# Performance work log

Hardware: AMD Instinct MI355X
Metric: run time of the kernel (lower is better)

Reference implementation:

```python
import jax, jax.numpy as jnp
import numpy as np

E = 2048
H = 16
DH = E // H  # 128
B, T = 2, 2048
EPS = 1e-8


def rmsnorm(x, g):
    rms = jnp.sqrt(jnp.mean(x * x, axis=-1, keepdims=True) + EPS)
    return g * (x / rms)


def setup_inputs() -> dict:
    key = jax.random.key(0)
    ks = jax.random.split(key, 16)
    s_in = 1.0 / np.sqrt(E)
    s_ff = 1.0 / np.sqrt(4 * E)
    return {
        "x": jax.random.normal(ks[0], (B, T, E), dtype=jnp.float32),
        # stacked per-head QKV projections, stored (in, out) so y = x @ W + b
        "wq": jax.random.normal(ks[1], (H, E, DH), dtype=jnp.float32) * s_in,
        "bq": jax.random.normal(ks[2], (H, DH), dtype=jnp.float32) * s_in,
        "wk": jax.random.normal(ks[3], (H, E, DH), dtype=jnp.float32) * s_in,
        "bk": jax.random.normal(ks[4], (H, DH), dtype=jnp.float32) * s_in,
        "wv": jax.random.normal(ks[5], (H, E, DH), dtype=jnp.float32) * s_in,
        "bv": jax.random.normal(ks[6], (H, DH), dtype=jnp.float32) * s_in,
        "wo": jax.random.normal(ks[7], (E, E), dtype=jnp.float32) * s_in,
        "bo": jax.random.normal(ks[8], (E,), dtype=jnp.float32) * s_in,
        "w1": jax.random.normal(ks[9], (E, 4 * E), dtype=jnp.float32) * s_in,
        "b1": jax.random.normal(ks[10], (4 * E,), dtype=jnp.float32) * s_in,
        "w2": jax.random.normal(ks[11], (4 * E, E), dtype=jnp.float32) * s_ff,
        "b2": jax.random.normal(ks[12], (E,), dtype=jnp.float32) * s_ff,
        "g1": jnp.ones((E,), dtype=jnp.float32),
        "g2": jnp.ones((E,), dtype=jnp.float32),
    }


def reference(x, wq, bq, wk, bk, wv, bv, wo, bo, w1, b1, w2, b2, g1, g2):
    b, t, e = x.shape
    # --- attention sublayer ---
    h = rmsnorm(x, g1)
    q = jnp.einsum("bte,hed->bhtd", h, wq) + bq[None, :, None, :]
    k = jnp.einsum("bte,hed->bhtd", h, wk) + bk[None, :, None, :]
    v = jnp.einsum("bte,hed->bhtd", h, wv) + bv[None, :, None, :]
    scores = jnp.einsum("bhtd,bhsd->bhts", q, k) / jnp.sqrt(jnp.float32(DH))
    causal = jnp.tril(jnp.ones((t, t), dtype=bool))
    scores = jnp.where(causal[None, None], scores, -jnp.inf)
    w = jax.nn.softmax(scores, axis=-1)
    o = jnp.einsum("bhts,bhsd->bhtd", w, v)
    o = o.transpose(0, 2, 1, 3).reshape(b, t, e)  # concat heads on last dim
    x = x + o @ wo + bo
    # --- FFN sublayer (exact GELU, dropout is identity at inference) ---
    h = rmsnorm(x, g2)
    x = x + jax.nn.gelu(h @ w1 + b1, approximate=False) @ w2 + b2
    return x
```

## Files before the change

kernel.cpp:

```cpp
#include <hip/hip_runtime.h>
#include <hip/hip_bf16.h>

typedef unsigned short u16;
typedef unsigned int   u32;
typedef __attribute__((ext_vector_type(8))) short short8;
typedef __attribute__((ext_vector_type(4))) float f32x4;
typedef __attribute__((ext_vector_type(4))) unsigned short u16x4;

#define E_    2048
#define H_    16
#define DH_   128
#define B_    2
#define T_    2048
#define NTOK  4096
#define QKVN  6144

#define VMCNT(n) asm volatile("s_waitcnt vmcnt(" #n ")" ::: "memory")
#define LGKM0()  asm volatile("s_waitcnt lgkmcnt(0)" ::: "memory")

__device__ __forceinline__ u16 f2bf(float f) {
  union { float f; u32 u; } v; v.f = f;
  u32 r = (v.u + 0x7FFFu + ((v.u >> 16) & 1u)) >> 16;
  return (u16)r;
}

__global__ __launch_bounds__(256) void tr64(
    const float* __restrict__ in, u16* __restrict__ out,
    int R, int C, size_t inZ, size_t outZ)
{
  __shared__ float t[64][65];
  const float* ib = in + (size_t)blockIdx.z * inZ;
  u16* ob = out + (size_t)blockIdx.z * outZ;
  const int r0 = blockIdx.y * 64, c0 = blockIdx.x * 64;
  const int tid = threadIdx.x;
  const int rr = tid >> 4;
  const int cc = (tid & 15) * 4;
  #pragma unroll
  for (int p = 0; p < 4; ++p) {
    const float4 v = *(const float4*)(ib + (size_t)(r0 + p * 16 + rr) * C + c0 + cc);
    t[cc + 0][p * 16 + rr] = v.x;
    t[cc + 1][p * 16 + rr] = v.y;
    t[cc + 2][p * 16 + rr] = v.z;
    t[cc + 3][p * 16 + rr] = v.w;
  }
  __syncthreads();
  const int wr = tid >> 3;
  const int wc = (tid & 7) * 8;
  #pragma unroll
  for (int p = 0; p < 2; ++p) {
    short8 s;
    #pragma unroll
    for (int j = 0; j < 8; ++j) s[j] = (short)f2bf(t[p * 32 + wr][wc + j]);
    *(short8*)(ob + (size_t)(c0 + p * 32 + wr) * R + r0 + wc) = s;
  }
}

__global__ __launch_bounds__(256) void bias_cat(
    const float* __restrict__ bq, const float* __restrict__ bk,
    const float* __restrict__ bv, float* __restrict__ bias)
{
  int idx = blockIdx.x * 256 + threadIdx.x;
  const float* bb = (idx < 2048) ? bq : (idx < 4096) ? bk : bv;
  bias[idx] = bb[idx & 2047];
}

__global__ __launch_bounds__(256) void rmsnorm_k(
    const float* __restrict__ x, const float* __restrict__ g, u16* __restrict__ o)
{
  const int row = blockIdx.x;
  const float4* xr = (const float4*)(x + (size_t)row * E_);
  const float4* gr = (const float4*)g;
  const int tid = threadIdx.x;
  float4 a0 = xr[tid], a1 = xr[tid + 256];
  float s = a0.x*a0.x + a0.y*a0.y + a0.z*a0.z + a0.w*a0.w
          + a1.x*a1.x + a1.y*a1.y + a1.z*a1.z + a1.w*a1.w;
  #pragma unroll
  for (int m = 1; m < 64; m <<= 1) s += __shfl_xor(s, m);
  __shared__ float wsum[4];
  if ((tid & 63) == 0) wsum[tid >> 6] = s;
  __syncthreads();
  float tot = wsum[0] + wsum[1] + wsum[2] + wsum[3];
  float rinv = rsqrtf(tot * (1.0f / E_) + 1e-8f);
  float4 g0 = gr[tid], g1 = gr[tid + 256];
  u16x4 o0, o1;
  o0[0] = f2bf(a0.x * g0.x * rinv); o0[1] = f2bf(a0.y * g0.y * rinv);
  o0[2] = f2bf(a0.z * g0.z * rinv); o0[3] = f2bf(a0.w * g0.w * rinv);
  o1[0] = f2bf(a1.x * g1.x * rinv); o1[1] = f2bf(a1.y * g1.y * rinv);
  o1[2] = f2bf(a1.z * g1.z * rinv); o1[3] = f2bf(a1.w * g1.w * rinv);
  u16x4* orow = (u16x4*)(o + (size_t)row * E_);
  orow[tid] = o0;
  orow[tid + 256] = o1;
}

__device__ __forceinline__ void gload_lds16(const void* g, u16* lds_base) {
  __builtin_amdgcn_global_load_lds(
      (const __attribute__((address_space(1))) u32*)g,
      (__attribute__((address_space(3))) u32*)lds_base, 16, 0, 0);
}

template<int BM, int BN, int MODE, int EPI>
__global__ __launch_bounds__(512, 2)
void gemm3(const u16* __restrict__ A, const u16* __restrict__ Bt,
           const float* __restrict__ bias, const float* __restrict__ resid,
           void* __restrict__ out, u16* __restrict__ vtout, int M, int N, int K)
{
  constexpr int WROWS = BM / 2;
  constexpr int WCOLS = BN / 4;
  constexpr int MR    = WROWS / 16;
  constexpr int BUF   = (BM + BN) * 32;
  __shared__ __align__(16) u16 sh[3 * BUF];

  const int tid  = threadIdx.x;
  const int lane = tid & 63;
  const int l15  = lane & 15, lg = lane >> 4;
  const int w    = tid >> 6;
  const int wm   = w >> 2;
  const int wn   = w & 3;
  const int xs   = (l15 >> 1) & 3;

  const int nbx = N / BN;
  const int xcd = blockIdx.x & 7, j = blockIdx.x >> 3;
  int m0, n0;
  if constexpr (MODE == 1) {
    const int ncx = nbx >> 3;
    n0 = (xcd * ncx + j % ncx) * BN;
    m0 = (j / ncx) * BM;
  } else {
    const int nwg = nbx * (M / BM);
    const int sid = xcd * (nwg >> 3) + j;
    m0 = (sid / nbx) * BM;
    n0 = (sid % nbx) * BN;
  }

  const int r0 = tid >> 2;
  const int c0 = (((tid & 3) ^ ((tid >> 3) & 3)) * 8);
  const u16* gA  = A  + (size_t)(m0 + r0) * K + c0;
  const u16* gB  = Bt + (size_t)(n0 + r0) * K + c0;
  const u16* gA2 = gA + (size_t)128 * K;
  const u16* gB2 = gB + (size_t)128 * K;
  const int wub = (tid & ~63) * 8;

  f32x4 acc[MR][4] = {};
  const int NT = K >> 5;

  #pragma unroll
  for (int t = 0; t < 2; ++t) {
    u16* wb = sh + t * BUF;
    const int kS = t * 32;
    if constexpr (BM == 256) {
      gload_lds16(gA  + kS, wb + wub);
      gload_lds16(gA2 + kS, wb + 4096 + wub);
      gload_lds16(gB  + kS, wb + 8192 + wub);
      gload_lds16(gB2 + kS, wb + 12288 + wub);
    } else {
      gload_lds16(gA  + kS, wb + wub);
      gload_lds16(gB  + kS, wb + 4096 + wub);
      gload_lds16(gB2 + kS, wb + 8192 + wub);
    }
  }
  if constexpr (BM == 256) VMCNT(4); else VMCNT(3);
  __builtin_amdgcn_s_barrier();

  int i = 0;

#define KTILE(CUR, STG)                                                          \
  do {                                                                           \
    const u16* rb = sh + (CUR) * BUF;                                            \
    u16* wb = sh + (STG) * BUF;                                                  \
    const bool st = (i + 2 < NT);                                                \
    const int kS = (i + 2) << 5;                                                 \
    const int rem = NT - 1 - i;                                                  \
    if (st) {                                                                    \
      if constexpr (BM == 256) {                                                 \
        gload_lds16(gA  + kS, wb + wub);                                         \
        gload_lds16(gA2 + kS, wb + 4096 + wub);                                  \
        gload_lds16(gB  + kS, wb + 8192 + wub);                                  \
        gload_lds16(gB2 + kS, wb + 12288 + wub);                                 \
      } else {                                                                   \
        gload_lds16(gA  + kS, wb + wub);                                         \
        gload_lds16(gB  + kS, wb + 4096 + wub);                                  \
        gload_lds16(gB2 + kS, wb + 8192 + wub);                                  \
      }                                                                          \
    }                                                                            \
    short8 bf[4];                                                                \
    _Pragma("unroll")                                                            \
    for (int n = 0; n < 4; ++n)                                                  \
      bf[n] = *(const short8*)(rb + BM * 32 + (wn * WCOLS + n * 16 + l15) * 32 + ((lg ^ xs) * 8)); \
    _Pragma("unroll")                                                            \
    for (int mh = 0; mh < MR / 4; ++mh) {                                        \
      short8 af[4];                                                              \
      _Pragma("unroll")                                                          \
      for (int m = 0; m < 4; ++m)                                                \
        af[m] = *(const short8*)(rb + (wm * WROWS + (mh * 4 + m) * 16 + l15) * 32 + ((lg ^ xs) * 8)); \
      _Pragma("unroll")                                                          \
      for (int m = 0; m < 4; ++m)                                                \
        _Pragma("unroll")                                                        \
        for (int n = 0; n < 4; ++n)                                              \
          acc[mh * 4 + m][n] = __builtin_amdgcn_mfma_f32_16x16x32_bf16(af[m], bf[n], acc[mh * 4 + m][n], 0, 0, 0); \
    }                                                                            \
    if (rem >= 2) { if constexpr (BM == 256) { VMCNT(4); } else { VMCNT(3); } }  \
    else { VMCNT(0); }                                                           \
    __builtin_amdgcn_s_barrier();                                                \
    ++i;                                                                         \
  } while (0)

  const int trips = NT / 3;
  #pragma unroll 1
  for (int t = 0; t < trips; ++t) {
    KTILE(0, 2);
    KTILE(1, 0);
    KTILE(2, 1);
  }
  if (i < NT) KTILE(0, 2);
  if (i < NT) KTILE(1, 0);
#undef KTILE

  float bv[4];
  #pragma unroll
  for (int n = 0; n < 4; ++n) bv[n] = bias[n0 + wn * WCOLS + n * 16 + l15];

  if constexpr (EPI == 1) {
    #pragma unroll
    for (int n = 0; n < 4; ++n) {
      const int col = n0 + wn * WCOLS + n * 16 + l15;
      #pragma unroll
      for (int m = 0; m < MR; ++m)
        #pragma unroll
        for (int r = 0; r < 4; ++r) {
          const int row = m0 + wm * WROWS + m * 16 + lg * 4 + r;
          const size_t off = (size_t)row * N + col;
          ((float*)out)[off] = acc[m][n][r] + bv[n] + resid[off];
        }
    }
  } else if (EPI == 3 && n0 >= 4096) {
    u16* epb = sh + w * 4096;
    #pragma unroll
    for (int n = 0; n < 4; ++n)
      #pragma unroll
      for (int m = 0; m < MR; ++m)
        #pragma unroll
        for (int r = 0; r < 4; ++r)
          epb[(n * 16 + l15) * 64 + m * 16 + lg * 4 + r] = f2bf(acc[m][n][r] + bv[n]);
    LGKM0();
    const int colV0 = n0 - 4096 + wn * 64;
    const int hh = colV0 >> 7;
    const int db = colV0 & 127;
    const int tw = m0 + wm * WROWS;
    const int bb = tw >> 11;
    const int tb = tw & 2047;
    u16* vbase = vtout + ((size_t)(bb * 16 + hh) * 128 + db) * 2048 + tb;
    #pragma unroll
    for (int it = 0; it < 8; ++it) {
      const int c = it * 64 + lane;
      const int d = c >> 3, sl = c & 7;
      short8 s = *(const short8*)(epb + d * 64 + sl * 8);
      *(short8*)(vbase + (size_t)d * 2048 + sl * 8) = s;
    }
  } else {
    u16* ep = sh + w * 1024;
    #pragma unroll
    for (int m = 0; m < MR; ++m) {
      #pragma unroll
      for (int n = 0; n < 4; ++n)
        #pragma unroll
        for (int r = 0; r < 4; ++r) {
          float v = acc[m][n][r] + bv[n];
          if (EPI == 2) {
            float t = v * (0.79788456080286536f + 0.0356774081363231f * v * v);
            v = v / (1.0f + __expf(-2.0f * t));
          }
          ep[(lg * 4 + r) * 64 + n * 16 + l15] = f2bf(v);
        }
      LGKM0();
      const int row0 = m0 + wm * WROWS + m * 16;
      #pragma unroll
      for (int it = 0; it < 2; ++it) {
        const int ch = it * 64 + lane;
        const int rr = ch >> 3, c8 = ch & 7;
        short8 s = *(const short8*)(ep + rr * 64 + c8 * 8);
        *(short8*)((u16*)out + (size_t)(row0 + rr) * N + n0 + wn * WCOLS + c8 * 8) = s;
      }
      LGKM0();
    }
  }
}

__global__ __launch_bounds__(256) void attn_k(
    const u16* __restrict__ qkv, const u16* __restrict__ vt, u16* __restrict__ o)
{
  const int tid  = threadIdx.x;
  const int lane = tid & 63;
  const int w    = tid >> 6;
  const int l15  = lane & 15, lg = lane >> 4;
  const int bid  = blockIdx.x;
  const int pair = bid & 31;
  const int qt   = 15 - (bid >> 5);
  const int h    = pair & 15;
  const int b    = pair >> 4;
  const int Q0 = qt * 128;
  const int qw = Q0 + w * 32;

  __shared__ __align__(16) u16 Ks[2][64 * 128];
  __shared__ __align__(16) u16 Vs[2][128 * 64];
  __shared__ __align__(16) u16 Ps[4][32 * 64];

  const u16* qb  = qkv + (size_t)b * T_ * QKVN + h * DH_;
  const u16* kb  = qb + E_;
  const u16* vtb = vt + (size_t)(b * H_ + h) * DH_ * T_;

  short8 qf[2][4];
  #pragma unroll
  for (int qi = 0; qi < 2; ++qi)
    #pragma unroll
    for (int kk = 0; kk < 4; ++kk)
      qf[qi][kk] = *(const short8*)(qb + (size_t)(qw + qi * 16 + l15) * QKVN + kk * 32 + lg * 8);

  f32x4 oacc[2][8] = {};
  float m_[2][4], l_[2][4];
  #pragma unroll
  for (int qi = 0; qi < 2; ++qi)
    #pragma unroll
    for (int r = 0; r < 4; ++r) { m_[qi][r] = -1e30f; l_[qi][r] = 0.f; }

  const int xr = l15 & 7;
  const float scl = 0.08838834764831845f;
  const int nt = Q0 / 64 + 2;
  const int qmaxw = qw + 31;
  const int wub = (tid & ~63);

  const u16* kp[4]; const u16* vp[4];
  #pragma unroll
  for (int i = 0; i < 4; ++i) {
    int f = i * 256 + tid;
    int r = f >> 4, p = f & 15, c = p ^ (r & 7);
    kp[i] = kb + (size_t)r * QKVN + c * 8;
  }
  #pragma unroll
  for (int i = 0; i < 4; ++i) {
    int f = i * 256 + tid;
    int d = f >> 3, p = f & 7, c = p ^ (d & 7);
    vp[i] = vtb + (size_t)d * T_ + c * 8;
  }

  auto STAGEKV = [&](int s0, int bufi) {
    const size_t ko = (size_t)s0 * QKVN;
    #pragma unroll
    for (int i = 0; i < 4; ++i)
      gload_lds16(kp[i] + ko, &Ks[bufi][(i * 256 + wub) * 8]);
    #pragma unroll
    for (int i = 0; i < 4; ++i)
      gload_lds16(vp[i] + s0, &Vs[bufi][(i * 256 + wub) * 8]);
  };

  STAGEKV(0, 0);
  VMCNT(0);
  __builtin_amdgcn_s_barrier();

  #pragma unroll 1
  for (int st = 0; st < nt; ++st) {
    const int s0 = st * 64;
    const int cur = st & 1;
    if (st + 1 < nt) STAGEKV(s0 + 64, cur ^ 1);

    if (s0 <= qmaxw) {
      const u16* Kc = Ks[cur];
      const u16* Vc = Vs[cur];
      f32x4 sc[2][4] = {};
      __builtin_amdgcn_s_setprio(1);
      #pragma unroll
      for (int sj = 0; sj < 4; ++sj) {
        const int row = sj * 16 + l15;
        #pragma unroll
        for (int kk = 0; kk < 4; ++kk) {
          short8 kfr = *(const short8*)(Kc + row * 128 + (((kk * 4 + lg) ^ xr) * 8));
          sc[0][sj] = __builtin_amdgcn_mfma_f32_16x16x32_bf16(qf[0][kk], kfr, sc[0][sj], 0, 0, 0);
          sc[1][sj] = __builtin_amdgcn_mfma_f32_16x16x32_bf16(qf[1][kk], kfr, sc[1][sj], 0, 0, 0);
        }
      }
      __builtin_amdgcn_s_setprio(0);
      const bool needmask = (s0 + 63 > qw);
      #pragma unroll
      for (int qi = 0; qi < 2; ++qi)
        #pragma unroll
        for (int sj = 0; sj < 4; ++sj)
          #pragma unroll
          for (int r = 0; r < 4; ++r) {
            float v = sc[qi][sj][r] * scl;
            if (needmask) {
              int s = s0 + sj * 16 + l15;
              int q = qw + qi * 16 + lg * 4 + r;
              if (s > q) v = -1e30f;
            }
            sc[qi][sj][r] = v;
          }
      #pragma unroll
      for (int qi = 0; qi < 2; ++qi) {
        float tmax[4], alpha[4], rsum[4];
        #pragma unroll
        for (int r = 0; r < 4; ++r)
          tmax[r] = fmaxf(fmaxf(sc[qi][0][r], sc[qi][1][r]), fmaxf(sc[qi][2][r], sc[qi][3][r]));
        #pragma unroll
        for (int r = 0; r < 4; ++r)
          #pragma unroll
          for (int m = 1; m < 16; m <<= 1) tmax[r] = fmaxf(tmax[r], __shfl_xor(tmax[r], m));
        #pragma unroll
        for (int r = 0; r < 4; ++r) {
          float mn = fmaxf(m_[qi][r], tmax[r]);
          alpha[r] = __expf(m_[qi][r] - mn);
          m_[qi][r] = mn;
          rsum[r] = 0.f;
        }
        #pragma unroll
        for (int sj = 0; sj < 4; ++sj)
          #pragma unroll
          for (int r = 0; r < 4; ++r) {
            float p = __expf(sc[qi][sj][r] - m_[qi][r]);
            rsum[r] += p;
            const int row = qi * 16 + lg * 4 + r;
            const int ch  = (sj * 2 + (l15 >> 3)) ^ (row & 7);
            Ps[w][row * 64 + ch * 8 + (l15 & 7)] = f2bf(p);
          }
        #pragma unroll
        for (int r = 0; r < 4; ++r) {
          #pragma unroll
          for (int m = 1; m < 16; m <<= 1) rsum[r] += __shfl_xor(rsum[r], m);
          l_[qi][r] = l_[qi][r] * alpha[r] + rsum[r];
        }
        #pragma unroll
        for (int dj = 0; dj < 8; ++dj)
          #pragma unroll
          for (int r = 0; r < 4; ++r) oacc[qi][dj][r] *= alpha[r];
      }
      __builtin_amdgcn_s_setprio(1);
      #pragma unroll
      for (int ks = 0; ks < 2; ++ks) {
        short8 pf0 = *(const short8*)(&Ps[w][l15 * 64 + (((ks * 4 + lg) ^ xr) * 8)]);
        short8 pf1 = *(const short8*)(&Ps[w][(16 + l15) * 64 + (((ks * 4 + lg) ^ xr) * 8)]);
        #pragma unroll
        for (int dj = 0; dj < 8; ++dj) {
          const int row = dj * 16 + l15;
          short8 vfr = *(const short8*)(Vc + row * 64 + (((ks * 4 + lg) ^ xr) * 8));
          oacc[0][dj] = __builtin_amdgcn_mfma_f32_16x16x32_bf16(pf0, vfr, oacc[0][dj], 0, 0, 0);
          oacc[1][dj] = __builtin_amdgcn_mfma_f32_16x16x32_bf16(pf1, vfr, oacc[1][dj], 0, 0, 0);
        }
      }
      __builtin_amdgcn_s_setprio(0);
    }
    VMCNT(0);
    __builtin_amdgcn_s_barrier();
  }

  float inv[2][4];
  #pragma unroll
  for (int qi = 0; qi < 2; ++qi)
    #pragma unroll
    for (int r = 0; r < 4; ++r) inv[qi][r] = 1.0f / l_[qi][r];
  u16* ob = o + (size_t)(b * T_ + qw) * E_ + h * DH_;
  #pragma unroll
  for (int qi = 0; qi < 2; ++qi)
    #pragma unroll
    for (int dj = 0; dj < 8; ++dj)
      #pragma unroll
      for (int r = 0; r < 4; ++r)
        ob[(size_t)(qi * 16 + lg * 4 + r) * E_ + dj * 16 + l15] = f2bf(oacc[qi][dj][r] * inv[qi][r]);
}

extern "C" void kernel_launch(void* const* d_in, const int* in_sizes, int n_in,
                              void* d_out, int out_size, void* d_ws, size_t ws_size,
                              hipStream_t stream)
{
  const float* x  = (const float*)d_in[0];
  const float* wq = (const float*)d_in[1];
  const float* bq = (const float*)d_in[2];
  const float* wk = (const float*)d_in[3];
  const float* bk = (const float*)d_in[4];
  const float* wv = (const float*)d_in[5];
  const float* bv = (const float*)d_in[6];
  const float* wo = (const float*)d_in[7];
  const float* bo = (const float*)d_in[8];
  const float* w1 = (const float*)d_in[9];
  const float* b1 = (const float*)d_in[10];
  const float* w2 = (const float*)d_in[11];
  const float* b2 = (const float*)d_in[12];
  const float* g1 = (const float*)d_in[13];
  const float* g2 = (const float*)d_in[14];
  float* xout = (float*)d_out;

  if (ws_size < 201351168u) return;

  char* ws = (char*)d_ws;
  u16*   wqkv_t = (u16*)(ws + 0);
  u16*   h1     = (u16*)(ws + 25165824);
  u16*   qkv    = (u16*)(ws + 41943040);
  u16*   vt     = (u16*)(ws + 92274688);
  u16*   o_     = (u16*)(ws + 109051904);
  u16*   wo_t   = (u16*)(ws + 125829120);
  u16*   w1_t   = (u16*)(ws + 134217728);
  u16*   w2_t   = (u16*)(ws + 167772160);
  float* bqkv   = (float*)(ws + 201326592);
  u16*   u_     = (u16*)(ws + 0);
  u16*   h2     = vt;
  float* x2     = xout;

  tr64<<<dim3(2, 32, 16), 256, 0, stream>>>(wq, wqkv_t,                          E_, DH_, (size_t)E_ * DH_, (size_t)DH_ * E_);
  tr64<<<dim3(2, 32, 16), 256, 0, stream>>>(wk, wqkv_t + (size_t)E_ * E_,        E_, DH_, (size_t)E_ * DH_, (size_t)DH_ * E_);
  tr64<<<dim3(2, 32, 16), 256, 0, stream>>>(wv, wqkv_t + (size_t)2 * E_ * E_,    E_, DH_, (size_t)E_ * DH_, (size_t)DH_ * E_);
  tr64<<<dim3(32, 32, 1),  256, 0, stream>>>(wo, wo_t, E_, E_, 0, 0);
  tr64<<<dim3(128, 32, 1), 256, 0, stream>>>(w1, w1_t, E_, 4 * E_, 0, 0);
  tr64<<<dim3(32, 128, 1), 256, 0, stream>>>(w2, w2_t, 4 * E_, E_, 0, 0);
  bias_cat<<<24, 256, 0, stream>>>(bq, bk, bv, bqkv);

  rmsnorm_k<<<NTOK, 256, 0, stream>>>(x, g1, h1);
  gemm3<128, 256, 1, 3><<<(NTOK / 128) * (QKVN / 256), 512, 0, stream>>>(h1, wqkv_t, bqkv, nullptr, qkv, vt, NTOK, QKVN, E_);
  attn_k<<<B_ * H_ * (T_ / 16 / 8), 256, 0, stream>>>(qkv, vt, o_);
  gemm3<128, 256, 0, 1><<<(NTOK / 128) * (E_ / 256), 512, 0, stream>>>(o_, wo_t, bo, x, x2, nullptr, NTOK, E_, E_);
  rmsnorm_k<<<NTOK, 256, 0, stream>>>(x2, g2, h2);
  gemm3<256, 256, 1, 2><<<(NTOK / 256) * (4 * E_ / 256), 512, 0, stream>>>(h2, w1_t, b1, nullptr, u_, nullptr, NTOK, 4 * E_, E_);
  gemm3<128, 256, 0, 1><<<(NTOK / 128) * (E_ / 256), 512, 0, stream>>>(u_, w2_t, b2, x2, xout, nullptr, NTOK, E_, 4 * E_);
}
```

Baseline: 667.3 us.

## Merge weight-prep launches into one kernel and add lazy softmax rescaling

Replaces the six transpose/convert launches and the bias concat with a single prep_all kernel that dispatches on block index, removing launch gaps and tail effects between the small prep kernels. Attention softmax now rescales the output accumulator and running sum only when some lane's tile max exceeds the running max by more than 8, so most tiles skip the exp and multiply of alpha. The threshold keeps unnormalized probabilities bounded by e^8 before the final division, which is accurate in fp32 but lets bf16 P values range wider.

```diff
diff --git a/kernel.cpp b/kernel.cpp
--- a/kernel.cpp
+++ b/kernel.cpp
@@ -24,15 +24,10 @@
   return (u16)r;
 }
 
-__global__ __launch_bounds__(256) void tr64(
-    const float* __restrict__ in, u16* __restrict__ out,
-    int R, int C, size_t inZ, size_t outZ)
+__device__ __forceinline__ void tr64_body(
+    const float* __restrict__ ib, u16* __restrict__ ob,
+    int R, int C, int r0, int c0, int tid, float (*t)[65])
 {
-  __shared__ float t[64][65];
-  const float* ib = in + (size_t)blockIdx.z * inZ;
-  u16* ob = out + (size_t)blockIdx.z * outZ;
-  const int r0 = blockIdx.y * 64, c0 = blockIdx.x * 64;
-  const int tid = threadIdx.x;
   const int rr = tid >> 4;
   const int cc = (tid & 15) * 4;
   #pragma unroll
@@ -55,13 +50,40 @@
   }
 }
 
-__global__ __launch_bounds__(256) void bias_cat(
-    const float* __restrict__ bq, const float* __restrict__ bk,
-    const float* __restrict__ bv, float* __restrict__ bias)
+__global__ __launch_bounds__(256) void prep_all(
+    const float* __restrict__ wq, const float* __restrict__ wk, const float* __restrict__ wv,
+    const float* __restrict__ wo, const float* __restrict__ w1, const float* __restrict__ w2,
+    const float* __restrict__ bq, const float* __restrict__ bk, const float* __restrict__ bv,
+    u16* __restrict__ wqkv_t, u16* __restrict__ wo_t, u16* __restrict__ w1_t, u16* __restrict__ w2_t,
+    float* __restrict__ bqkv)
 {
-  int idx = blockIdx.x * 256 + threadIdx.x;
-  const float* bb = (idx < 2048) ? bq : (idx < 4096) ? bk : bv;
-  bias[idx] = bb[idx & 2047];
+  __shared__ float t[64][65];
+  const int bid = blockIdx.x;
+  const int tid = threadIdx.x;
+  if (bid < 3072) {
+    const int sec = bid >> 10;
+    const int tI  = bid & 1023;
+    const int z   = tI >> 6;
+    const int by  = (tI >> 1) & 31;
+    const int bx  = tI & 1;
+    const float* src = (sec == 0) ? wq : (sec == 1) ? wk : wv;
+    tr64_body(src + (size_t)z * E_ * DH_,
+              wqkv_t + (size_t)sec * E_ * E_ + (size_t)z * DH_ * E_,
+              E_, DH_, by * 64, bx * 64, tid, t);
+  } else if (bid < 4096) {
+    const int tI = bid - 3072;
+    tr64_body(wo, wo_t, E_, E_, (tI >> 5) * 64, (tI & 31) * 64, tid, t);
+  } else if (bid < 8192) {
+    const int tI = bid - 4096;
+    tr64_body(w1, w1_t, E_, 4 * E_, (tI >> 7) * 64, (tI & 127) * 64, tid, t);
+  } else if (bid < 12288) {
+    const int tI = bid - 8192;
+    tr64_body(w2, w2_t, 4 * E_, E_, (tI >> 5) * 64, (tI & 31) * 64, tid, t);
+  } else {
+    const int idx = (bid - 12288) * 256 + tid;
+    const float* bb = (idx < 2048) ? bq : (idx < 4096) ? bk : bv;
+    bqkv[idx] = bb[idx & 2047];
+  }
 }
 
 __global__ __launch_bounds__(256) void rmsnorm_k(
@@ -393,23 +415,41 @@
             }
             sc[qi][sj][r] = v;
           }
+      float tmax[2][4];
       #pragma unroll
       for (int qi = 0; qi < 2; ++qi) {
-        float tmax[4], alpha[4], rsum[4];
-        #pragma unroll
-        for (int r = 0; r < 4; ++r)
-          tmax[r] = fmaxf(fmaxf(sc[qi][0][r], sc[qi][1][r]), fmaxf(sc[qi][2][r], sc[qi][3][r]));
-        #pragma unroll
-        for (int r = 0; r < 4; ++r)
+        #pragma unroll
+        for (int r = 0; r < 4; ++r) {
+          tmax[qi][r] = fmaxf(fmaxf(sc[qi][0][r], sc[qi][1][r]), fmaxf(sc[qi][2][r], sc[qi][3][r]));
           #pragma unroll
-          for (int m = 1; m < 16; m <<= 1) tmax[r] = fmaxf(tmax[r], __shfl_xor(tmax[r], m));
-        #pragma unroll
-        for (int r = 0; r < 4; ++r) {
-          float mn = fmaxf(m_[qi][r], tmax[r]);
-          alpha[r] = __expf(m_[qi][r] - mn);
-          m_[qi][r] = mn;
-          rsum[r] = 0.f;
-        }
+          for (int m = 1; m < 16; m <<= 1) tmax[qi][r] = fmaxf(tmax[qi][r], __shfl_xor(tmax[qi][r], m));
+        }
+      }
+      bool grow = false;
+      #pragma unroll
+      for (int qi = 0; qi < 2; ++qi)
+        #pragma unroll
+        for (int r = 0; r < 4; ++r) grow |= (tmax[qi][r] > m_[qi][r] + 8.0f);
+      if (__any(grow)) {
+        #pragma unroll
+        for (int qi = 0; qi < 2; ++qi) {
+          float alpha[4];
+          #pragma unroll
+          for (int r = 0; r < 4; ++r) {
+            float mn = fmaxf(m_[qi][r], tmax[qi][r]);
+            alpha[r] = __expf(m_[qi][r] - mn);
+            m_[qi][r] = mn;
+            l_[qi][r] *= alpha[r];
+          }
+          #pragma unroll
+          for (int dj = 0; dj < 8; ++dj)
+            #pragma unroll
+            for (int r = 0; r < 4; ++r) oacc[qi][dj][r] *= alpha[r];
+        }
+      }
+      #pragma unroll
+      for (int qi = 0; qi < 2; ++qi) {
+        float rsum[4] = {0.f, 0.f, 0.f, 0.f};
         #pragma unroll
         for (int sj = 0; sj < 4; ++sj)
           #pragma unroll
@@ -424,12 +464,8 @@
         for (int r = 0; r < 4; ++r) {
           #pragma unroll
           for (int m = 1; m < 16; m <<= 1) rsum[r] += __shfl_xor(rsum[r], m);
-          l_[qi][r] = l_[qi][r] * alpha[r] + rsum[r];
-        }
-        #pragma unroll
-        for (int dj = 0; dj < 8; ++dj)
-          #pragma unroll
-          for (int r = 0; r < 4; ++r) oacc[qi][dj][r] *= alpha[r];
+          l_[qi][r] += rsum[r];
+        }
       }
       __builtin_amdgcn_s_setprio(1);
       #pragma unroll
@@ -502,13 +538,8 @@
   u16*   h2     = vt;
   float* x2     = xout;
 
-  tr64<<<dim3(2, 32, 16), 256, 0, stream>>>(wq, wqkv_t,                          E_, DH_, (size_t)E_ * DH_, (size_t)DH_ * E_);
-  tr64<<<dim3(2, 32, 16), 256, 0, stream>>>(wk, wqkv_t + (size_t)E_ * E_,        E_, DH_, (size_t)E_ * DH_, (size_t)DH_ * E_);
-  tr64<<<dim3(2, 32, 16), 256, 0, stream>>>(wv, wqkv_t + (size_t)2 * E_ * E_,    E_, DH_, (size_t)E_ * DH_, (size_t)DH_ * E_);
-  tr64<<<dim3(32, 32, 1),  256, 0, stream>>>(wo, wo_t, E_, E_, 0, 0);
-  tr64<<<dim3(128, 32, 1), 256, 0, stream>>>(w1, w1_t, E_, 4 * E_, 0, 0);
-  tr64<<<dim3(32, 128, 1), 256, 0, stream>>>(w2, w2_t, 4 * E_, E_, 0, 0);
-  bias_cat<<<24, 256, 0, stream>>>(bq, bk, bv, bqkv);
+  prep_all<<<12312, 256, 0, stream>>>(wq, wk, wv, wo, w1, w2, bq, bk, bv,
+                                      wqkv_t, wo_t, w1_t, w2_t, bqkv);
 
   rmsnorm_k<<<NTOK, 256, 0, stream>>>(x, g1, h1);
   gemm3<128, 256, 1, 3><<<(NTOK / 128) * (QKVN / 256), 512, 0, stream>>>(h1, wqkv_t, bqkv, nullptr, qkv, vt, NTOK, QKVN, E_);
```

After: 652.6 us. -2.2%, faster.
